# Kernel tuning notes

Measured on AMD Instinct MI355X. Metric: run time of the kernel, lower is better.

## Reference

```python
import jax, jax.numpy as jnp
import numpy as np

B, T, D, H, WIN, G = 2, 2048, 768, 12, 16, 32
HD = D // H            # 64
K = 2 * WIN + 1        # local kernel size = 33


def setup_inputs() -> dict:
    key = jax.random.key(0)
    ks = jax.random.split(key, 5)
    s = 1.0 / np.sqrt(D).astype(np.float32)
    x = jax.random.normal(ks[0], (B, T, D), jnp.float32)
    # first G tokens of every batch are global (matches original's nonzero(global_mask[b]))
    global_mask = jnp.zeros((B, T), jnp.int32).at[:, :G].set(1)
    Wq = jax.random.normal(ks[1], (D, D), jnp.float32) * s
    Wk = jax.random.normal(ks[2], (D, D), jnp.float32) * s
    Wv = jax.random.normal(ks[3], (D, D), jnp.float32) * s
    Wo = jax.random.normal(ks[4], (D, D), jnp.float32) * s
    bq = jnp.zeros((D,), jnp.float32)
    bk = jnp.zeros((D,), jnp.float32)
    bv = jnp.zeros((D,), jnp.float32)
    bo = jnp.zeros((D,), jnp.float32)
    return {"x": x, "global_mask": global_mask, "Wq": Wq, "bq": bq,
            "Wk": Wk, "bk": bk, "Wv": Wv, "bv": bv, "Wo": Wo, "bo": bo}


def reference(x, global_mask, Wq, bq, Wk, bk, Wv, bv, Wo, bo):
    def split_heads(y):
        return y.reshape(B, T, H, HD).transpose(0, 2, 1, 3)  # [B,H,T,HD]

    q = split_heads(x @ Wq + bq)
    k = split_heads(x @ Wk + bk)
    v = split_heads(x @ Wv + bv)

    scale = 1.0 / np.sqrt(HD).astype(np.float32)

    offs = jnp.arange(-WIN, WIN + 1)
    idx = jnp.arange(T)[:, None] + offs[None, :]          # [T,K]
    valid = (idx >= 0) & (idx < T)                        # [T,K]
    idxc = jnp.clip(idx, 0, T - 1)

    k_loc = k[:, :, idxc]                                 # [B,H,T,K,HD]
    s_loc = jnp.einsum('bhtd,bhtkd->bhtk', q, k_loc) * scale
    s_loc = jnp.where(valid, s_loc, -jnp.inf)             # out-of-range excluded from softmax

    # global tokens (same positions for every batch by construction)
    g_idx = jnp.nonzero(global_mask[0], size=G)[0]        # [G]
    k_g = k[:, :, g_idx]                                  # [B,H,G,HD]
    v_g = v[:, :, g_idx]
    s_g = jnp.einsum('bhtd,bhgd->bhtg', q, k_g) * scale   # [B,H,T,G]

    # joint softmax over [local window, global tokens] (globals in window are double-counted,
    # exactly as in the original torch.cat([local_s, g_score]))
    attn = jax.nn.softmax(jnp.concatenate([s_loc, s_g], axis=-1), axis=-1)
    a_loc = jnp.where(valid, attn[..., :K], 0.0)          # [B,H,T,K]
    a_g = attn[..., K:]                                   # [B,H,T,G]

    v_loc = v[:, :, idxc]                                 # [B,H,T,K,HD]
    ctx = (jnp.einsum('bhtk,bhtkd->bhtd', a_loc, v_loc)
           + jnp.einsum('bhtg,bhgd->bhtd', a_g, v_g))     # [B,H,T,HD]

    out = ctx.transpose(0, 2, 1, 3).reshape(B, T, D) @ Wo + bo

    # dense attention map: scatter local band (add; invalid entries are 0),
    # then overwrite global columns (matches original write order)
    rows = jnp.arange(T)[:, None]                         # [T,1]
    full_attn = jnp.zeros((B, H, T, T), jnp.float32)
    full_attn = full_attn.at[:, :, rows, idxc].add(a_loc)
    full_attn = full_attn.at[:, :, :, g_idx].set(a_g)
    return out, full_attn
```

## Files before the change

### kernel.cpp

```cpp
#include <hip/hip_runtime.h>

typedef unsigned short u16;
typedef __attribute__((ext_vector_type(4))) u16 u16x4;
typedef __attribute__((ext_vector_type(8))) u16 u16x8;
typedef __attribute__((ext_vector_type(8))) short bf16x8;
typedef __attribute__((ext_vector_type(4))) float f32x4;

#define BB 2
#define TT 2048
#define DD 768
#define NH 12
#define HDIM 64
#define NQKV 2304
#define MM 4096

__device__ __forceinline__ u16 f2bf(float f) {
  unsigned u = __float_as_uint(f);
  u += 0x7fffu + ((u >> 16) & 1u);
  return (u16)(u >> 16);
}
__device__ __forceinline__ float bf2f(u16 s) {
  return __uint_as_float(((unsigned)s) << 16);
}
__device__ __forceinline__ void async_load16(const void* g, void* l) {
  __builtin_amdgcn_global_load_lds((const __attribute__((address_space(1))) void*)g,
                                   (__attribute__((address_space(3))) void*)l, 16, 0, 0);
}

__global__ __launch_bounds__(256) void castx(const float* __restrict__ x, u16* __restrict__ xb) {
  int i = blockIdx.x * 256 + threadIdx.x;
  float4 v = ((const float4*)x)[i];
  u16x4 o = { f2bf(v.x), f2bf(v.y), f2bf(v.z), f2bf(v.w) };
  ((u16x4*)xb)[i] = o;
}

__global__ __launch_bounds__(256) void wprep(const float* __restrict__ Wq, const float* __restrict__ Wk,
                                             const float* __restrict__ Wv, const float* __restrict__ Wo,
                                             u16* __restrict__ wqkvT, u16* __restrict__ woT) {
  __shared__ float tile[32][33];
  int z = blockIdx.z;
  const float* W = (z == 0) ? Wq : (z == 1) ? Wk : (z == 2) ? Wv : Wo;
  u16* dst = (z < 3) ? (wqkvT + (size_t)z * DD * DD) : woT;
  int k0 = blockIdx.x * 32, n0 = blockIdx.y * 32;
  int tx = threadIdx.x, ty = threadIdx.y;
#pragma unroll
  for (int j = 0; j < 4; ++j)
    tile[ty + j * 8][tx] = W[(size_t)(k0 + ty + j * 8) * DD + n0 + tx];
  __syncthreads();
#pragma unroll
  for (int j = 0; j < 4; ++j)
    dst[(size_t)(n0 + ty + j * 8) * DD + k0 + tx] = f2bf(tile[tx][ty + j * 8]);
}

__global__ __launch_bounds__(64) void prep_misc(const int* __restrict__ gm,
                                                const float* __restrict__ bq, const float* __restrict__ bk,
                                                const float* __restrict__ bv,
                                                int* __restrict__ gidx, int* __restrict__ gpos,
                                                float* __restrict__ biasqkv) {
  int lane = threadIdx.x;
  if (lane < 32) gidx[lane] = 0;
  for (int c = lane; c < TT; c += 64) gpos[c] = -1;
  int base = 0;
  for (int c0 = 0; c0 < TT; c0 += 64) {
    int mval = gm[c0 + lane];
    unsigned long long bal = __ballot(mval != 0);
    int pre = __popcll(bal & ((1ull << lane) - 1ull));
    if (mval && (base + pre) < 32) { gidx[base + pre] = c0 + lane; gpos[c0 + lane] = base + pre; }
    base += __popcll(bal);
  }
  for (int n = lane; n < NQKV; n += 64)
    biasqkv[n] = (n < 768) ? bq[n] : (n < 1536) ? bk[n - 768] : bv[n - 1536];
}

__global__ __launch_bounds__(256) void gemm_bt(const u16* __restrict__ A, const u16* __restrict__ BT,
                                               const float* __restrict__ bias, float* __restrict__ C,
                                               int Mdim, int Ndim, int Kd) {
  __shared__ __attribute__((aligned(16))) u16 As[128 * 64];
  __shared__ __attribute__((aligned(16))) u16 Bs[128 * 64];
  const int tid = threadIdx.x;
  const int wave = tid >> 6, lane = tid & 63;
  const int m0 = blockIdx.x * 128, n0 = blockIdx.y * 128;
  const int wm = (wave & 1) << 6, wn = (wave >> 1) << 6;
  const int lr = lane & 15, lk = lane >> 4;
  const int srow_b = lane >> 3;
  const int scol = (lane & 7) * 8;

  f32x4 acc[4][4] = {};

  const int kIters = Kd >> 6;
  for (int kt = 0; kt < kIters; ++kt) {
#pragma unroll
    for (int cc = 0; cc < 4; ++cc) {
      int c = wave * 4 + cc;
      int srow = c * 8 + srow_b;
      async_load16(A + (size_t)(m0 + srow) * Kd + (kt << 6) + scol, (void*)(As + c * 512));
      async_load16(BT + (size_t)(n0 + srow) * Kd + (kt << 6) + scol, (void*)(Bs + c * 512));
    }
    __syncthreads();
#pragma unroll
    for (int kc = 0; kc < 2; ++kc) {
      bf16x8 af[4], bfr[4];
#pragma unroll
      for (int i = 0; i < 4; ++i)
        af[i] = *(const bf16x8*)(As + (wm + i * 16 + lr) * 64 + kc * 32 + lk * 8);
#pragma unroll
      for (int j = 0; j < 4; ++j)
        bfr[j] = *(const bf16x8*)(Bs + (wn + j * 16 + lr) * 64 + kc * 32 + lk * 8);
#pragma unroll
      for (int i = 0; i < 4; ++i)
#pragma unroll
        for (int j = 0; j < 4; ++j)
          acc[i][j] = __builtin_amdgcn_mfma_f32_16x16x32_bf16(af[i], bfr[j], acc[i][j], 0, 0, 0);
    }
    __syncthreads();
  }

#pragma unroll
  for (int i = 0; i < 4; ++i) {
    const int row = m0 + wm + i * 16 + lk * 4;
#pragma unroll
    for (int j = 0; j < 4; ++j) {
      const int col = n0 + wn + j * 16 + lr;
      const float bs = bias[col];
#pragma unroll
      for (int r = 0; r < 4; ++r)
        C[(size_t)(row + r) * Ndim + col] = acc[i][j][r] + bs;
    }
  }
}

__global__ __launch_bounds__(256) void attn_kernel(const float* __restrict__ qkv,
                                                   const int* __restrict__ gidx,
                                                   const int* __restrict__ gpos,
                                                   u16* __restrict__ ctxb,
                                                   float* __restrict__ fattn) {
  __shared__ __attribute__((aligned(16))) u16 Kl[96 * 72];
  __shared__ __attribute__((aligned(16))) u16 Kg[32 * 72];
  __shared__ __attribute__((aligned(16))) u16 Vl[96 * 72];
  __shared__ __attribute__((aligned(16))) u16 Vg[32 * 72];
  __shared__ __attribute__((aligned(16))) float probs[64 * 68];
  __shared__ int gposs[TT];

  const int tid = threadIdx.x;
  const int blk = blockIdx.x;
  const int chunk = blk & 31;
  const int h = (blk >> 5) % NH;
  const int b = blk / 384;
  const int t0 = chunk << 6;

  {
    const int r = tid >> 4;
    const int c4 = (tid & 15) << 2;
#pragma unroll
    for (int it = 0; it < 6; ++it) {
      int rr = it * 16 + r;
      int t = t0 - 16 + rr;
      t = t < 0 ? 0 : (t > TT - 1 ? TT - 1 : t);
      const float* src = qkv + (size_t)(b * TT + t) * NQKV + h * HDIM;
      float4 kv = *(const float4*)(src + 768 + c4);
      float4 vv = *(const float4*)(src + 1536 + c4);
      u16x4 kb = { f2bf(kv.x), f2bf(kv.y), f2bf(kv.z), f2bf(kv.w) };
      u16x4 vb = { f2bf(vv.x), f2bf(vv.y), f2bf(vv.z), f2bf(vv.w) };
      *(u16x4*)(Kl + rr * 72 + c4) = kb;
      *(u16x4*)(Vl + rr * 72 + c4) = vb;
    }
#pragma unroll
    for (int it = 0; it < 2; ++it) {
      int rr = it * 16 + r;
      int t = gidx[rr];
      const float* src = qkv + (size_t)(b * TT + t) * NQKV + h * HDIM;
      float4 kv = *(const float4*)(src + 768 + c4);
      float4 vv = *(const float4*)(src + 1536 + c4);
      u16x4 kb = { f2bf(kv.x), f2bf(kv.y), f2bf(kv.z), f2bf(kv.w) };
      u16x4 vb = { f2bf(vv.x), f2bf(vv.y), f2bf(vv.z), f2bf(vv.w) };
      *(u16x4*)(Kg + rr * 72 + c4) = kb;
      *(u16x4*)(Vg + rr * 72 + c4) = vb;
    }
    for (int i = tid; i < TT; i += 256) gposs[i] = gpos[i];
  }
  __syncthreads();

  const int tl = tid >> 2, sub = tid & 3;
  const int t = t0 + tl;
  const float* qp = qkv + (size_t)(b * TT + t) * NQKV + h * HDIM;
  float4 qr[16];
#pragma unroll
  for (int i = 0; i < 16; ++i) qr[i] = ((const float4*)qp)[i];

  float sc[17], pe[17];
  float mmax = -__builtin_inff();
#pragma unroll
  for (int i = 0; i < 17; ++i) {
    const int s = sub + (i << 2);
    const u16* kp;
    bool valid;
    if (s < 33) { kp = Kl + (tl + s) * 72; int j = t - 16 + s; valid = (j >= 0) && (j < TT); }
    else if (s < 65) { kp = Kg + (s - 33) * 72; valid = true; }
    else { kp = Kg; valid = false; }
    float d = 0.f;
#pragma unroll
    for (int i2 = 0; i2 < 8; ++i2) {
      u16x8 kv = *(const u16x8*)(kp + i2 * 8);
      float4 qa = qr[i2 * 2], qb = qr[i2 * 2 + 1];
      d += qa.x * bf2f(kv[0]) + qa.y * bf2f(kv[1]) + qa.z * bf2f(kv[2]) + qa.w * bf2f(kv[3]);
      d += qb.x * bf2f(kv[4]) + qb.y * bf2f(kv[5]) + qb.z * bf2f(kv[6]) + qb.w * bf2f(kv[7]);
    }
    sc[i] = valid ? d * 0.125f : -__builtin_inff();
    mmax = fmaxf(mmax, sc[i]);
  }
  mmax = fmaxf(mmax, __shfl_xor(mmax, 1));
  mmax = fmaxf(mmax, __shfl_xor(mmax, 2));
  float sum = 0.f;
#pragma unroll
  for (int i = 0; i < 17; ++i) { pe[i] = __expf(sc[i] - mmax); sum += pe[i]; }
  sum += __shfl_xor(sum, 1);
  sum += __shfl_xor(sum, 2);
  const float inv = 1.0f / sum;
#pragma unroll
  for (int i = 0; i < 17; ++i) {
    const int s = sub + (i << 2);
    if (s < 65) probs[tl * 68 + s] = pe[i] * inv;
  }
  __syncthreads();

  float cacc[16];
#pragma unroll
  for (int i = 0; i < 16; ++i) cacc[i] = 0.f;
#pragma unroll 1
  for (int k = 0; k < 65; ++k) {
    const float pv = probs[tl * 68 + k];
    const u16* vp = (k < 33) ? (Vl + (tl + k) * 72) : (Vg + (k - 33) * 72);
    const u16* vq = vp + (sub << 4);
    u16x8 v0 = *(const u16x8*)(vq);
    u16x8 v1 = *(const u16x8*)(vq + 8);
#pragma unroll
    for (int e = 0; e < 8; ++e) { cacc[e] += pv * bf2f(v0[e]); cacc[8 + e] += pv * bf2f(v1[e]); }
  }
  {
    u16x8 cb0, cb1;
#pragma unroll
    for (int e = 0; e < 8; ++e) { cb0[e] = f2bf(cacc[e]); cb1[e] = f2bf(cacc[8 + e]); }
    u16* dst = ctxb + (size_t)(b * TT + t) * DD + h * HDIM + (sub << 4);
    *(u16x8*)dst = cb0;
    *(u16x8*)(dst + 8) = cb1;
  }

  float* fbase = fattn + (size_t)(b * NH + h) * TT * TT;
#pragma unroll 1
  for (int it = 0; it < 128; ++it) {
    int f = it * 256 + tid;
    int rl = f >> 9;
    int c4 = (f & 511) << 2;
    const float* pr = probs + rl * 68;
    int trow = t0 + rl;
    float vals[4];
#pragma unroll
    for (int e = 0; e < 4; ++e) {
      int c = c4 + e;
      float val = 0.f;
      int kk = c - trow + 16;
      if ((unsigned)kk < 33u) val = pr[kk];
      int g = gposs[c];
      if (g >= 0) val = pr[33 + g];
      vals[e] = val;
    }
    *(float4*)(fbase + (size_t)trow * TT + c4) = make_float4(vals[0], vals[1], vals[2], vals[3]);
  }
}

extern "C" void kernel_launch(void* const* d_in, const int* in_sizes, int n_in,
                              void* d_out, int out_size, void* d_ws, size_t ws_size,
                              hipStream_t stream) {
  const float* x  = (const float*)d_in[0];
  const int* gm   = (const int*)d_in[1];
  const float* Wq = (const float*)d_in[2];
  const float* bq = (const float*)d_in[3];
  const float* Wk = (const float*)d_in[4];
  const float* bk = (const float*)d_in[5];
  const float* Wv = (const float*)d_in[6];
  const float* bv = (const float*)d_in[7];
  const float* Wo = (const float*)d_in[8];
  const float* bo = (const float*)d_in[9];

  float* out = (float*)d_out;
  float* fattn = out + (size_t)BB * TT * DD;

  char* p = (char*)d_ws;
  u16* xb      = (u16*)p;  p += (size_t)MM * DD * 2;
  u16* wqkvT   = (u16*)p;  p += (size_t)NQKV * DD * 2;
  u16* woT     = (u16*)p;  p += (size_t)DD * DD * 2;
  float* biasq = (float*)p; p += (size_t)NQKV * 4;
  int* gidx    = (int*)p;  p += 128;
  int* gpos    = (int*)p;  p += (size_t)TT * 4;
  float* qkv   = (float*)p; p += (size_t)MM * NQKV * 4;
  u16* ctxb    = (u16*)p;  p += (size_t)MM * DD * 2;

  castx<<<MM * DD / 4 / 256, 256, 0, stream>>>(x, xb);
  wprep<<<dim3(24, 24, 4), dim3(32, 8), 0, stream>>>(Wq, Wk, Wv, Wo, wqkvT, woT);
  prep_misc<<<1, 64, 0, stream>>>(gm, bq, bk, bv, gidx, gpos, biasq);
  gemm_bt<<<dim3(MM / 128, NQKV / 128), 256, 0, stream>>>(xb, wqkvT, biasq, qkv, MM, NQKV, DD);
  attn_kernel<<<BB * NH * (TT / 64), 256, 0, stream>>>(qkv, gidx, gpos, ctxb, fattn);
  gemm_bt<<<dim3(MM / 128, DD / 128), 256, 0, stream>>>(ctxb, woT, bo, out, MM, DD, DD);
}
```

Measured before the change: 636.9 us.

## Zero-fill dense attention map separately and scatter only band and global entries

The dense attention map is now cleared by a dedicated vectorized fill kernel, and the attention kernel writes only the band and global-column probabilities directly from registers. Before, it built every full row from shared memory using per-column gpos lookups. The aim is to take the large row-construction work and the full-TT gpos shared copy out of the attention kernel, at the cost of scattered scalar stores. The output projection GEMM also switches to 64-row tiles so it launches more blocks, and prep_misc uses 256 threads with an early exit.

```diff
diff --git a/kernel.cpp b/kernel.cpp
--- a/kernel.cpp
+++ b/kernel.cpp
@@ -25,6 +25,10 @@
 __device__ __forceinline__ void async_load16(const void* g, void* l) {
   __builtin_amdgcn_global_load_lds((const __attribute__((address_space(1))) void*)g,
                                    (__attribute__((address_space(3))) void*)l, 16, 0, 0);
+}
+
+__global__ __launch_bounds__(256) void fill0(float4* __restrict__ p) {
+  p[(size_t)blockIdx.x * 256 + threadIdx.x] = make_float4(0.f, 0.f, 0.f, 0.f);
 }
 
 __global__ __launch_bounds__(256) void castx(const float* __restrict__ x, u16* __restrict__ xb) {
@@ -52,64 +56,78 @@
     dst[(size_t)(n0 + ty + j * 8) * DD + k0 + tx] = f2bf(tile[tx][ty + j * 8]);
 }
 
-__global__ __launch_bounds__(64) void prep_misc(const int* __restrict__ gm,
-                                                const float* __restrict__ bq, const float* __restrict__ bk,
-                                                const float* __restrict__ bv,
-                                                int* __restrict__ gidx, int* __restrict__ gpos,
-                                                float* __restrict__ biasqkv) {
-  int lane = threadIdx.x;
-  if (lane < 32) gidx[lane] = 0;
-  for (int c = lane; c < TT; c += 64) gpos[c] = -1;
-  int base = 0;
-  for (int c0 = 0; c0 < TT; c0 += 64) {
-    int mval = gm[c0 + lane];
-    unsigned long long bal = __ballot(mval != 0);
-    int pre = __popcll(bal & ((1ull << lane) - 1ull));
-    if (mval && (base + pre) < 32) { gidx[base + pre] = c0 + lane; gpos[c0 + lane] = base + pre; }
-    base += __popcll(bal);
-  }
-  for (int n = lane; n < NQKV; n += 64)
+__global__ __launch_bounds__(256) void prep_misc(const int* __restrict__ gm,
+                                                 const float* __restrict__ bq, const float* __restrict__ bk,
+                                                 const float* __restrict__ bv,
+                                                 int* __restrict__ gidx, int* __restrict__ gpos,
+                                                 float* __restrict__ biasqkv) {
+  int tid = threadIdx.x;
+  if (tid < 32) gidx[tid] = 0;
+  for (int c = tid; c < TT; c += 256) gpos[c] = -1;
+  for (int n = tid; n < NQKV; n += 256)
     biasqkv[n] = (n < 768) ? bq[n] : (n < 1536) ? bk[n - 768] : bv[n - 1536];
-}
-
+  __syncthreads();
+  if (tid < 64) {
+    int lane = tid;
+    int base = 0;
+    for (int c0 = 0; c0 < TT; c0 += 64) {
+      int mval = gm[c0 + lane];
+      unsigned long long bal = __ballot(mval != 0);
+      int pre = __popcll(bal & ((1ull << lane) - 1ull));
+      if (mval && (base + pre) < 32) { gidx[base + pre] = c0 + lane; gpos[c0 + lane] = base + pre; }
+      base += __popcll(bal);
+      if (base >= 32) break;
+    }
+  }
+}
+
+template <int BM>
 __global__ __launch_bounds__(256) void gemm_bt(const u16* __restrict__ A, const u16* __restrict__ BT,
                                                const float* __restrict__ bias, float* __restrict__ C,
-                                               int Mdim, int Ndim, int Kd) {
-  __shared__ __attribute__((aligned(16))) u16 As[128 * 64];
+                                               int Ndim, int Kd) {
+  constexpr int NJ = (BM == 128) ? 4 : 2;
+  constexpr int ACH = BM / 32;
+  __shared__ __attribute__((aligned(16))) u16 As[BM * 64];
   __shared__ __attribute__((aligned(16))) u16 Bs[128 * 64];
   const int tid = threadIdx.x;
   const int wave = tid >> 6, lane = tid & 63;
-  const int m0 = blockIdx.x * 128, n0 = blockIdx.y * 128;
-  const int wm = (wave & 1) << 6, wn = (wave >> 1) << 6;
+  const int m0 = blockIdx.x * BM, n0 = blockIdx.y * 128;
+  const int wm = (BM == 128) ? ((wave & 1) << 6) : 0;
+  const int wn = (BM == 128) ? ((wave >> 1) << 6) : (wave << 5);
   const int lr = lane & 15, lk = lane >> 4;
   const int srow_b = lane >> 3;
   const int scol = (lane & 7) * 8;
 
-  f32x4 acc[4][4] = {};
+  f32x4 acc[4][NJ] = {};
 
   const int kIters = Kd >> 6;
   for (int kt = 0; kt < kIters; ++kt) {
+#pragma unroll
+    for (int cc = 0; cc < ACH; ++cc) {
+      int c = wave * ACH + cc;
+      int srow = c * 8 + srow_b;
+      async_load16(A + (size_t)(m0 + srow) * Kd + (kt << 6) + scol, (void*)(As + c * 512));
+    }
 #pragma unroll
     for (int cc = 0; cc < 4; ++cc) {
       int c = wave * 4 + cc;
       int srow = c * 8 + srow_b;
-      async_load16(A + (size_t)(m0 + srow) * Kd + (kt << 6) + scol, (void*)(As + c * 512));
       async_load16(BT + (size_t)(n0 + srow) * Kd + (kt << 6) + scol, (void*)(Bs + c * 512));
     }
     __syncthreads();
 #pragma unroll
     for (int kc = 0; kc < 2; ++kc) {
-      bf16x8 af[4], bfr[4];
+      bf16x8 af[4], bfr[NJ];
 #pragma unroll
       for (int i = 0; i < 4; ++i)
         af[i] = *(const bf16x8*)(As + (wm + i * 16 + lr) * 64 + kc * 32 + lk * 8);
 #pragma unroll
-      for (int j = 0; j < 4; ++j)
+      for (int j = 0; j < NJ; ++j)
         bfr[j] = *(const bf16x8*)(Bs + (wn + j * 16 + lr) * 64 + kc * 32 + lk * 8);
 #pragma unroll
       for (int i = 0; i < 4; ++i)
 #pragma unroll
-        for (int j = 0; j < 4; ++j)
+        for (int j = 0; j < NJ; ++j)
           acc[i][j] = __builtin_amdgcn_mfma_f32_16x16x32_bf16(af[i], bfr[j], acc[i][j], 0, 0, 0);
     }
     __syncthreads();
@@ -119,7 +137,7 @@
   for (int i = 0; i < 4; ++i) {
     const int row = m0 + wm + i * 16 + lk * 4;
 #pragma unroll
-    for (int j = 0; j < 4; ++j) {
+    for (int j = 0; j < NJ; ++j) {
       const int col = n0 + wn + j * 16 + lr;
       const float bs = bias[col];
 #pragma unroll
@@ -139,7 +157,8 @@
   __shared__ __attribute__((aligned(16))) u16 Vl[96 * 72];
   __shared__ __attribute__((aligned(16))) u16 Vg[32 * 72];
   __shared__ __attribute__((aligned(16))) float probs[64 * 68];
-  __shared__ int gposs[TT];
+  __shared__ int wgpos[96];
+  __shared__ int gidxs[32];
 
   const int tid = threadIdx.x;
   const int blk = blockIdx.x;
@@ -176,7 +195,11 @@
       *(u16x4*)(Kg + rr * 72 + c4) = kb;
       *(u16x4*)(Vg + rr * 72 + c4) = vb;
     }
-    for (int i = tid; i < TT; i += 256) gposs[i] = gpos[i];
+    if (tid < 32) gidxs[tid] = gidx[tid];
+    if (tid < 96) {
+      int t = t0 - 16 + tid;
+      wgpos[tid] = ((unsigned)t < TT) ? gpos[t] : -1;
+    }
   }
   __syncthreads();
 
@@ -187,7 +210,7 @@
 #pragma unroll
   for (int i = 0; i < 16; ++i) qr[i] = ((const float4*)qp)[i];
 
-  float sc[17], pe[17];
+  float sc[17];
   float mmax = -__builtin_inff();
 #pragma unroll
   for (int i = 0; i < 17; ++i) {
@@ -212,14 +235,15 @@
   mmax = fmaxf(mmax, __shfl_xor(mmax, 2));
   float sum = 0.f;
 #pragma unroll
-  for (int i = 0; i < 17; ++i) { pe[i] = __expf(sc[i] - mmax); sum += pe[i]; }
+  for (int i = 0; i < 17; ++i) { sc[i] = __expf(sc[i] - mmax); sum += sc[i]; }
   sum += __shfl_xor(sum, 1);
   sum += __shfl_xor(sum, 2);
   const float inv = 1.0f / sum;
 #pragma unroll
   for (int i = 0; i < 17; ++i) {
     const int s = sub + (i << 2);
-    if (s < 65) probs[tl * 68 + s] = pe[i] * inv;
+    sc[i] *= inv;
+    if (s < 65) probs[tl * 68 + s] = sc[i];
   }
   __syncthreads();
 
@@ -245,26 +269,17 @@
     *(u16x8*)(dst + 8) = cb1;
   }
 
-  float* fbase = fattn + (size_t)(b * NH + h) * TT * TT;
-#pragma unroll 1
-  for (int it = 0; it < 128; ++it) {
-    int f = it * 256 + tid;
-    int rl = f >> 9;
-    int c4 = (f & 511) << 2;
-    const float* pr = probs + rl * 68;
-    int trow = t0 + rl;
-    float vals[4];
-#pragma unroll
-    for (int e = 0; e < 4; ++e) {
-      int c = c4 + e;
-      float val = 0.f;
-      int kk = c - trow + 16;
-      if ((unsigned)kk < 33u) val = pr[kk];
-      int g = gposs[c];
-      if (g >= 0) val = pr[33 + g];
-      vals[e] = val;
-    }
-    *(float4*)(fbase + (size_t)trow * TT + c4) = make_float4(vals[0], vals[1], vals[2], vals[3]);
+  float* frow = fattn + ((size_t)(b * NH + h) * TT + t) * TT;
+#pragma unroll
+  for (int i = 0; i < 17; ++i) {
+    const int s = sub + (i << 2);
+    const float p = sc[i];
+    if (s < 33) {
+      int c = t - 16 + s;
+      if ((unsigned)c < TT && wgpos[tl + s] < 0) frow[c] = p;
+    } else if (s < 65) {
+      frow[gidxs[s - 33]] = p;
+    }
   }
 }
 
@@ -297,8 +312,9 @@
 
   castx<<<MM * DD / 4 / 256, 256, 0, stream>>>(x, xb);
   wprep<<<dim3(24, 24, 4), dim3(32, 8), 0, stream>>>(Wq, Wk, Wv, Wo, wqkvT, woT);
-  prep_misc<<<1, 64, 0, stream>>>(gm, bq, bk, bv, gidx, gpos, biasq);
-  gemm_bt<<<dim3(MM / 128, NQKV / 128), 256, 0, stream>>>(xb, wqkvT, biasq, qkv, MM, NQKV, DD);
+  prep_misc<<<1, 256, 0, stream>>>(gm, bq, bk, bv, gidx, gpos, biasq);
+  fill0<<<(size_t)BB * NH * TT * TT / 4 / 256, 256, 0, stream>>>((float4*)fattn);
+  gemm_bt<128><<<dim3(MM / 128, NQKV / 128), 256, 0, stream>>>(xb, wqkvT, biasq, qkv, NQKV, DD);
   attn_kernel<<<BB * NH * (TT / 64), 256, 0, stream>>>(qkv, gidx, gpos, ctxb, fattn);
-  gemm_bt<<<dim3(MM / 128, DD / 128), 256, 0, stream>>>(ctxb, woT, bo, out, MM, DD, DD);
-}
+  gemm_bt<64><<<dim3(MM / 64, DD / 128), 256, 0, stream>>>(ctxb, woT, bo, out, DD, DD);
+}
```

New measurement: 562.7 us. -11.7%, faster.
